# Performance work log

Hardware: AMD Instinct MI355X
Metric: run time of the kernel (lower is better)

The kernel has to match this reference:

```python
import math
import jax, jax.numpy as jnp
import numpy as np

IN_CH = 512
KEY = 512
VAL = 512
B, T = 8, 2048
SQRT_KEY = math.sqrt(float(KEY))


def setup_inputs() -> dict:
    key = jax.random.key(0)
    ks = jax.random.split(key, 7)
    s_in = 1.0 / math.sqrt(IN_CH)
    return {
        "x": jax.random.normal(ks[0], (B, T, IN_CH), dtype=jnp.float32),
        "Wq": jax.random.uniform(ks[1], (IN_CH, KEY), jnp.float32, -s_in, s_in),
        "bq": jax.random.uniform(ks[2], (KEY,), jnp.float32, -s_in, s_in),
        "Wk": jax.random.uniform(ks[3], (IN_CH, KEY), jnp.float32, -s_in, s_in),
        "bk": jax.random.uniform(ks[4], (KEY,), jnp.float32, -s_in, s_in),
        "Wv": jax.random.uniform(ks[5], (IN_CH, VAL), jnp.float32, -s_in, s_in),
        "bv": jax.random.uniform(ks[6], (VAL,), jnp.float32, -s_in, s_in),
    }


def reference(x, Wq, bq, Wk, bk, Wv, bv):
    # x: [B, T, C]
    q = x @ Wq + bq          # [B, T, K]
    k = x @ Wk + bk          # [B, T, K]
    v = x @ Wv + bv          # [B, T, V]
    logits = jnp.einsum("btk,bsk->bts", q, k)  # [B, T(q), T(kv)]
    mask = jnp.tril(jnp.ones((T, T), dtype=bool))  # causal: key s <= query t
    logits = jnp.where(mask[None, :, :], logits, -jnp.inf)
    # NOTE: original torch code softmaxes over dim=1 (the QUERY axis) — kept faithful.
    probs = jax.nn.softmax(logits / SQRT_KEY, axis=1)
    read = jnp.einsum("bts,bsv->btv", probs, v)  # [B, T, V]
    return jnp.concatenate((x, read), axis=2)    # [B, T, C+V]
```

## Files before the change

### kernel.cpp

```cpp
#include <hip/hip_runtime.h>
#include <hip/hip_bf16.h>
#include <math.h>

#define BATCH 8
#define SEQ   2048
#define CH    512
#define ROWS  (BATCH * SEQ)
#define INVSQ 0.044194173824159216f

#define BM 128
#define BK 32
#define TILE_ELEMS (BM * BK)
#define TP 68

typedef __attribute__((ext_vector_type(8))) __bf16 bf16x8;
typedef __attribute__((ext_vector_type(4))) float f32x4;

__device__ inline unsigned short f2bf(float f) {
    unsigned u = __builtin_bit_cast(unsigned, f);
    u += 0x7fffu + ((u >> 16) & 1u);
    return (unsigned short)(u >> 16);
}
__device__ inline float bf2f(unsigned short s) {
    unsigned u = ((unsigned)s) << 16;
    return __builtin_bit_cast(float, u);
}

__device__ __forceinline__ void stage_tile(
    const unsigned short* __restrict__ gbase, size_t stride,
    unsigned short* lds, int wave, int lane)
{
#pragma unroll
    for (int j = 0; j < 2; ++j) {
        int chunk = wave * 2 + j;
        int row = chunk * 16 + (lane >> 2);
        const unsigned short* g = gbase + (size_t)row * stride + ((lane & 3) << 3);
        __builtin_amdgcn_global_load_lds(
            (const __attribute__((address_space(1))) unsigned int*)g,
            (__attribute__((address_space(3))) unsigned int*)(lds + (chunk << 9)),
            16, 0, 0);
    }
}

__device__ __forceinline__ void load_frags(
    const unsigned short* lds, int w0, int l16, int quad, bf16x8* f)
{
#pragma unroll
    for (int r = 0; r < 4; ++r)
        f[r] = *(const bf16x8*)(lds + (w0 + r * 16 + l16) * BK + quad * 8);
}

__global__ __launch_bounds__(256) void fuse_x_kernel(
    const float* __restrict__ x, unsigned short* __restrict__ xb,
    float* __restrict__ out, float* __restrict__ Z)
{
    if (blockIdx.x < 64) Z[blockIdx.x * 256 + threadIdx.x] = 0.f;
    size_t base = ((size_t)blockIdx.x * 256 + threadIdx.x) * 8;
    size_t row = base >> 9, c = base & 511;
    float4 v0 = *(const float4*)(x + base);
    float4 v1 = *(const float4*)(x + base + 4);
    float* o = out + row * 1024 + c;
    *(float4*)o = v0;
    *(float4*)(o + 4) = v1;
    alignas(16) unsigned short t[8];
    t[0] = f2bf(v0.x); t[1] = f2bf(v0.y); t[2] = f2bf(v0.z); t[3] = f2bf(v0.w);
    t[4] = f2bf(v1.x); t[5] = f2bf(v1.y); t[6] = f2bf(v1.z); t[7] = f2bf(v1.w);
    *(uint4*)(xb + base) = *(const uint4*)t;
}

__global__ __launch_bounds__(256) void transpose_w_kernel(
    const float* __restrict__ Wq, const float* __restrict__ Wk,
    const float* __restrict__ Wv, unsigned short* __restrict__ Wt)
{
    __shared__ unsigned short T[64 * TP];
    const int k0 = blockIdx.x * 64, n0 = blockIdx.y * 64, w = blockIdx.z;
    const float* W = (w == 0) ? Wq : (w == 1) ? Wk : Wv;
    const int tid = threadIdx.x;
#pragma unroll
    for (int i = 0; i < 2; ++i) {
        int slot = tid + i * 256;
        int kr = slot >> 3, c8 = (slot & 7) << 3;
        float4 a = *(const float4*)(W + (size_t)(k0 + kr) * CH + n0 + c8);
        float4 b = *(const float4*)(W + (size_t)(k0 + kr) * CH + n0 + c8 + 4);
        T[(c8 + 0) * TP + kr] = f2bf(a.x); T[(c8 + 1) * TP + kr] = f2bf(a.y);
        T[(c8 + 2) * TP + kr] = f2bf(a.z); T[(c8 + 3) * TP + kr] = f2bf(a.w);
        T[(c8 + 4) * TP + kr] = f2bf(b.x); T[(c8 + 5) * TP + kr] = f2bf(b.y);
        T[(c8 + 6) * TP + kr] = f2bf(b.z); T[(c8 + 7) * TP + kr] = f2bf(b.w);
    }
    __syncthreads();
#pragma unroll
    for (int i = 0; i < 2; ++i) {
        int slot = tid + i * 256;
        int nr = slot >> 3, k8 = (slot & 7) << 3;
        uint2 lo = *(const uint2*)(T + nr * TP + k8);
        uint2 hi = *(const uint2*)(T + nr * TP + k8 + 4);
        uint4 u; u.x = lo.x; u.y = lo.y; u.z = hi.x; u.w = hi.y;
        *(uint4*)(Wt + ((size_t)w * CH + n0 + nr) * CH + k0 + k8) = u;
    }
}

__global__ __launch_bounds__(256) void transpose_v_kernel(
    const unsigned short* __restrict__ vb, const float* __restrict__ Z,
    unsigned short* __restrict__ Vt)
{
    __shared__ unsigned short T[64 * TP];
    const int s0 = blockIdx.x * 64, v0 = blockIdx.y * 64, b = blockIdx.z;
    const int tid = threadIdx.x;
#pragma unroll
    for (int i = 0; i < 2; ++i) {
        int slot = tid + i * 256;
        int sr = slot >> 3, c8 = (slot & 7) << 3;
        float inv = 1.0f / Z[b * SEQ + s0 + sr];
        uint4 raw = *(const uint4*)(vb + ((size_t)b * SEQ + s0 + sr) * CH + v0 + c8);
        const unsigned short* p = (const unsigned short*)&raw;
#pragma unroll
        for (int j = 0; j < 8; ++j)
            T[(c8 + j) * TP + sr] = f2bf(bf2f(p[j]) * inv);
    }
    __syncthreads();
#pragma unroll
    for (int i = 0; i < 2; ++i) {
        int slot = tid + i * 256;
        int vr = slot >> 3, s8 = (slot & 7) << 3;
        uint2 lo = *(const uint2*)(T + vr * TP + s8);
        uint2 hi = *(const uint2*)(T + vr * TP + s8 + 4);
        uint4 u; u.x = lo.x; u.y = lo.y; u.z = hi.x; u.w = hi.y;
        *(uint4*)(Vt + ((size_t)b * CH + v0 + vr) * SEQ + s0 + s8) = u;
    }
}

#define MFMA_ROW(r, af) \
    acc[r][0] = __builtin_amdgcn_mfma_f32_16x16x32_bf16(af, b0, acc[r][0], 0, 0, 0); \
    acc[r][1] = __builtin_amdgcn_mfma_f32_16x16x32_bf16(af, b1, acc[r][1], 0, 0, 0); \
    acc[r][2] = __builtin_amdgcn_mfma_f32_16x16x32_bf16(af, b2, acc[r][2], 0, 0, 0); \
    acc[r][3] = __builtin_amdgcn_mfma_f32_16x16x32_bf16(af, b3, acc[r][3], 0, 0, 0);

__global__ __launch_bounds__(512, 2) void qkv8_kernel(
    const unsigned short* __restrict__ xb, const unsigned short* __restrict__ Wt,
    const float* __restrict__ bq, const float* __restrict__ bk,
    const float* __restrict__ bv, unsigned short* __restrict__ qkv)
{
    __shared__ unsigned short lds[24576];
    const int tid = threadIdx.x;
    const int lane = tid & 63, wave = tid >> 6;
    const int waveA = wave >> 2;
    const int waveB = wave & 3;
    const int quad = lane >> 4, l16 = lane & 15;

    int id = (int)blockIdx.x;
    id = (id & 7) * 96 + (id >> 3);
    const int xt = id / 12, wt = id - xt * 12;
    const int xrow0 = xt << 8, wrow0 = wt << 7;

    const unsigned short* __restrict__ Wg = Wt + (size_t)wrow0 * CH;
    const unsigned short* __restrict__ Xg = xb + (size_t)xrow0 * CH;

    const int srow = tid >> 2;
    const int scol = (((tid & 3) ^ ((tid >> 3) & 3)) << 3);
    const size_t ga  = (size_t)srow * CH + scol;
    const size_t gb1 = (size_t)(srow + 128) * CH + scol;
    const int wdst = wave * 512;
    const int rswz = ((quad ^ ((l16 >> 1) & 3)) << 3);
    const int arow = waveA * 64 + l16;
    const int brow = waveB * 64 + l16;

    f32x4 acc[4][4] = {};

    auto stageA = [&](int V) {
        if (V >= 16) return;
        const unsigned short* g = Wg + ga + V * 32;
        unsigned short* d = lds + (V & 1) * 4096 + wdst;
        __builtin_amdgcn_global_load_lds(
            (const __attribute__((address_space(1))) unsigned int*)g,
            (__attribute__((address_space(3))) unsigned int*)d, 16, 0, 0);
    };
    auto stageB = [&](int V) {
        if (V >= 16) return;
        const unsigned short* g0 = Xg + ga + V * 32;
        const unsigned short* g1 = Xg + gb1 + V * 32;
        unsigned short* d = lds + 8192 + (V & 1) * 8192 + wdst;
        __builtin_amdgcn_global_load_lds(
            (const __attribute__((address_space(1))) unsigned int*)g0,
            (__attribute__((address_space(3))) unsigned int*)d, 16, 0, 0);
        __builtin_amdgcn_global_load_lds(
            (const __attribute__((address_space(1))) unsigned int*)g1,
            (__attribute__((address_space(3))) unsigned int*)(d + 4096), 16, 0, 0);
    };

    stageA(0); stageB(0); stageB(1);
    asm volatile("s_waitcnt vmcnt(2)" ::: "memory");
    __builtin_amdgcn_s_barrier();
    __builtin_amdgcn_sched_barrier(0);

#pragma unroll
    for (int U = 0; U < 16; ++U) {
        const unsigned short* Ab = lds + (U & 1) * 4096;
        const unsigned short* Bb = lds + 8192 + (U & 1) * 8192;
        bf16x8 a0, a1, b0, b1, b2, b3;
        b0 = *(const bf16x8*)(Bb + (brow +  0) * 32 + rswz);
        b1 = *(const bf16x8*)(Bb + (brow + 16) * 32 + rswz);
        b2 = *(const bf16x8*)(Bb + (brow + 32) * 32 + rswz);
        b3 = *(const bf16x8*)(Bb + (brow + 48) * 32 + rswz);
        a0 = *(const bf16x8*)(Ab + (arow +  0) * 32 + rswz);
        a1 = *(const bf16x8*)(Ab + (arow + 16) * 32 + rswz);
        stageA(U + 1);
        __builtin_amdgcn_s_barrier();
        asm volatile("s_waitcnt lgkmcnt(0)" ::: "memory");
        __builtin_amdgcn_sched_barrier(0);
        __builtin_amdgcn_s_setprio(1);
        MFMA_ROW(0, a0);
        MFMA_ROW(1, a1);
        __builtin_amdgcn_s_setprio(0);
        __builtin_amdgcn_s_barrier();
        __builtin_amdgcn_sched_barrier(0);
        a0 = *(const bf16x8*)(Ab + (arow + 32) * 32 + rswz);
        a1 = *(const bf16x8*)(Ab + (arow + 48) * 32 + rswz);
        stageB(U + 2);
        __builtin_amdgcn_s_barrier();
        asm volatile("s_waitcnt lgkmcnt(0)" ::: "memory");
        __builtin_amdgcn_sched_barrier(0);
        __builtin_amdgcn_s_setprio(1);
        MFMA_ROW(2, a0);
        MFMA_ROW(3, a1);
        __builtin_amdgcn_s_setprio(0);
        if (U <= 13)      asm volatile("s_waitcnt vmcnt(2)" ::: "memory");
        else if (U == 14) asm volatile("s_waitcnt vmcnt(0)" ::: "memory");
        __builtin_amdgcn_s_barrier();
        __builtin_amdgcn_sched_barrier(0);
    }

    const int which = wrow0 >> 9;
    const float* bias = (which == 0) ? bq : (which == 1) ? bk : bv;
    const float scale = (which == 0) ? INVSQ : 1.0f;
    unsigned short* outw = qkv + (size_t)which * ROWS * CH;
    const int colblk = wrow0 & 511;
#pragma unroll
    for (int r = 0; r < 4; ++r) {
        int colb = colblk + waveA * 64 + r * 16 + quad * 4;
        float4 b4 = *(const float4*)(bias + colb);
#pragma unroll
        for (int c = 0; c < 4; ++c) {
            int m = xrow0 + waveB * 64 + c * 16 + l16;
            alignas(8) unsigned short pk[4];
            pk[0] = f2bf((acc[r][c][0] + b4.x) * scale);
            pk[1] = f2bf((acc[r][c][1] + b4.y) * scale);
            pk[2] = f2bf((acc[r][c][2] + b4.z) * scale);
            pk[3] = f2bf((acc[r][c][3] + b4.w) * scale);
            *(uint2*)(outw + (size_t)m * CH + colb) = *(const uint2*)pk;
        }
    }
}
#undef MFMA_ROW

__global__ __launch_bounds__(256) void logits_kernel(
    const unsigned short* __restrict__ qb, const unsigned short* __restrict__ kb,
    unsigned short* __restrict__ E, float* __restrict__ Z)
{
    __shared__ unsigned short As[2 * TILE_ELEMS];
    __shared__ unsigned short Bs[2 * TILE_ELEMS];
    const int id = blockIdx.x;
    const int b = id & 7;
    const int i = id >> 3;
    int tt = (int)((sqrtf(8.f * (float)i + 1.f) - 1.f) * 0.5f);
    int st = i - ((tt * (tt + 1)) >> 1);
    while (st < 0)  { --tt; st = i - ((tt * (tt + 1)) >> 1); }
    while (st > tt) { ++tt; st = i - ((tt * (tt + 1)) >> 1); }
    const int m0s = st * BM;
    const int n0t = tt * BM;
    const int tid = threadIdx.x;
    const int lane = tid & 63, wave = tid >> 6;
    const int wm = (wave >> 1) * 64, wn = (wave & 1) * 64;
    const int quad = lane >> 4, l16 = lane & 15;
    const unsigned short* kB = kb + (size_t)b * SEQ * CH;
    const unsigned short* qB = qb + (size_t)b * SEQ * CH;

    f32x4 acc[4][4] = {};
    for (int kk = 0; kk < CH; kk += 64) {
        stage_tile(kB + (size_t)m0s * CH + kk,      CH, As,              wave, lane);
        stage_tile(kB + (size_t)m0s * CH + kk + 32, CH, As + TILE_ELEMS, wave, lane);
        stage_tile(qB + (size_t)n0t * CH + kk,      CH, Bs,              wave, lane);
        stage_tile(qB + (size_t)n0t * CH + kk + 32, CH, Bs + TILE_ELEMS, wave, lane);
        __syncthreads();
#pragma unroll
        for (int h = 0; h < 2; ++h) {
            bf16x8 a[4], bb[4];
            load_frags(As + h * TILE_ELEMS, wm, l16, quad, a);
            load_frags(Bs + h * TILE_ELEMS, wn, l16, quad, bb);
#pragma unroll
            for (int r = 0; r < 4; ++r)
#pragma unroll
                for (int c = 0; c < 4; ++c)
                    acc[r][c] = __builtin_amdgcn_mfma_f32_16x16x32_bf16(a[r], bb[c], acc[r][c], 0, 0, 0);
        }
        __syncthreads();
    }
#pragma unroll
    for (int r = 0; r < 4; ++r) {
        int sb = m0s + wm + r * 16 + quad * 4;
        float ev[4][4];
#pragma unroll
        for (int c = 0; c < 4; ++c) {
            int t = n0t + wn + c * 16 + l16;
#pragma unroll
            for (int reg = 0; reg < 4; ++reg)
                ev[c][reg] = (sb + reg <= t) ? __expf(acc[r][c][reg]) : 0.f;
        }
#pragma unroll
        for (int reg = 0; reg < 4; ++reg) {
            float z = ev[0][reg] + ev[1][reg] + ev[2][reg] + ev[3][reg];
            z += __shfl_xor(z, 1);
            z += __shfl_xor(z, 2);
            z += __shfl_xor(z, 4);
            z += __shfl_xor(z, 8);
            if (l16 == 0) atomicAdd(&Z[b * SEQ + sb + reg], z);
        }
#pragma unroll
        for (int c = 0; c < 4; ++c) {
            int t = n0t + wn + c * 16 + l16;
            alignas(8) unsigned short pk[4];
            pk[0] = f2bf(ev[c][0]); pk[1] = f2bf(ev[c][1]);
            pk[2] = f2bf(ev[c][2]); pk[3] = f2bf(ev[c][3]);
            *(uint2*)(E + ((size_t)b * SEQ + t) * SEQ + sb) = *(const uint2*)pk;
        }
    }
}

__global__ __launch_bounds__(256) void read_kernel(
    const unsigned short* __restrict__ E, const unsigned short* __restrict__ Vt,
    float* __restrict__ out)
{
    __shared__ unsigned short As[2 * TILE_ELEMS];
    __shared__ unsigned short Bs[2 * TILE_ELEMS];
    const int id = blockIdx.x;
    const int b = id & 7;
    const int rem = id >> 3;
    const int mv = rem & 3;
    const int r0 = rem >> 2;
    const int tt = (r0 < 8) ? r0 : 23 - r0;
    const int m0v = mv * BM;
    const int n0t = tt * BM;
    const int Kmax = (tt + 1) * BM;
    const int tid = threadIdx.x;
    const int lane = tid & 63, wave = tid >> 6;
    const int wm = (wave >> 1) * 64, wn = (wave & 1) * 64;
    const int quad = lane >> 4, l16 = lane & 15;
    const unsigned short* Vb = Vt + (size_t)b * CH * SEQ;
    const unsigned short* Eb = E + (size_t)b * SEQ * SEQ;

    f32x4 acc[4][4] = {};
    for (int kk = 0; kk < Kmax; kk += 64) {
        stage_tile(Vb + (size_t)m0v * SEQ + kk,      SEQ, As,              wave, lane);
        stage_tile(Vb + (size_t)m0v * SEQ + kk + 32, SEQ, As + TILE_ELEMS, wave, lane);
        stage_tile(Eb + (size_t)n0t * SEQ + kk,      SEQ, Bs,              wave, lane);
        stage_tile(Eb + (size_t)n0t * SEQ + kk + 32, SEQ, Bs + TILE_ELEMS, wave, lane);
        __syncthreads();
#pragma unroll
        for (int h = 0; h < 2; ++h) {
            bf16x8 a[4], bb[4];
            load_frags(As + h * TILE_ELEMS, wm, l16, quad, a);
            load_frags(Bs + h * TILE_ELEMS, wn, l16, quad, bb);
#pragma unroll
            for (int r = 0; r < 4; ++r)
#pragma unroll
                for (int c = 0; c < 4; ++c)
                    acc[r][c] = __builtin_amdgcn_mfma_f32_16x16x32_bf16(a[r], bb[c], acc[r][c], 0, 0, 0);
        }
        __syncthreads();
    }
#pragma unroll
    for (int r = 0; r < 4; ++r) {
        int v = 512 + m0v + wm + r * 16 + quad * 4;
#pragma unroll
        for (int c = 0; c < 4; ++c) {
            int t = n0t + wn + c * 16 + l16;
            float4 f;
            f.x = acc[r][c][0]; f.y = acc[r][c][1];
            f.z = acc[r][c][2]; f.w = acc[r][c][3];
            *(float4*)(out + ((size_t)b * SEQ + t) * 1024 + v) = f;
        }
    }
}

extern "C" void kernel_launch(void* const* d_in, const int* in_sizes, int n_in,
                              void* d_out, int out_size, void* d_ws, size_t ws_size,
                              hipStream_t stream) {
    const float* x  = (const float*)d_in[0];
    const float* Wq = (const float*)d_in[1];
    const float* bq = (const float*)d_in[2];
    const float* Wk = (const float*)d_in[3];
    const float* bk = (const float*)d_in[4];
    const float* Wv = (const float*)d_in[5];
    const float* bv = (const float*)d_in[6];
    float* out = (float*)d_out;

    char* ws = (char*)d_ws;
    const size_t QKV_BYTES = (size_t)ROWS * CH * 2;
    const size_t E_BYTES   = (size_t)BATCH * SEQ * SEQ * 2;
    unsigned short* qkv = (unsigned short*)ws;
    unsigned short* qb = qkv;
    unsigned short* kb = (unsigned short*)(ws + QKV_BYTES);
    unsigned short* vb = (unsigned short*)(ws + 2 * QKV_BYTES);
    unsigned short* E  = (unsigned short*)(ws + 3 * QKV_BYTES);
    float* Z = (float*)(ws + 3 * QKV_BYTES + E_BYTES);
    unsigned short* xb = E;
    unsigned short* Wt = (unsigned short*)((char*)E + QKV_BYTES);
    unsigned short* Vt = qb;

    dim3 blk(256);
    fuse_x_kernel<<<dim3(4096), blk, 0, stream>>>(x, xb, out, Z);
    transpose_w_kernel<<<dim3(8, 8, 3), blk, 0, stream>>>(Wq, Wk, Wv, Wt);
    qkv8_kernel<<<dim3(768), dim3(512), 0, stream>>>(xb, Wt, bq, bk, bv, qkv);
    logits_kernel<<<dim3(1088), blk, 0, stream>>>(qb, kb, E, Z);
    transpose_v_kernel<<<dim3(32, 8, 8), blk, 0, stream>>>(vb, Z, Vt);
    read_kernel<<<dim3(512), blk, 0, stream>>>(E, Vt, out);
}
```

Measured before the change: 230.0 us.

## Port logits kernel to pipelined 8-wave async-LDS GEMM with 128x256 tiles

Replaces the simple 4-wave 128x128 logits GEMM, which stages tiles synchronously, with the same 8-wave, 512-thread pipeline used by the QKV projection. That pipeline uses double-buffered global_load_lds staging, barrier-interleaved MFMA phases and setprio, and covers 128 key rows by 256 query rows. The causal tile enumeration changes to 128x256 blocks, 576 in place of 1088, and the pipeline loop is factored into a shared macro. This aims to hide global-load latency and improve operand reuse in the QK^T stage. The cost is coarser tiles that do more wasted work on the masked triangle, and fewer blocks to spread across the CUs.

```diff
diff --git a/kernel.cpp b/kernel.cpp
--- a/kernel.cpp
+++ b/kernel.cpp
@@ -135,6 +135,48 @@
     acc[r][2] = __builtin_amdgcn_mfma_f32_16x16x32_bf16(af, b2, acc[r][2], 0, 0, 0); \
     acc[r][3] = __builtin_amdgcn_mfma_f32_16x16x32_bf16(af, b3, acc[r][3], 0, 0, 0);
 
+#define PIPELINE_LOOP                                                         \
+    stageA(0); stageB(0); stageB(1);                                          \
+    asm volatile("s_waitcnt vmcnt(2)" ::: "memory");                          \
+    __builtin_amdgcn_s_barrier();                                             \
+    __builtin_amdgcn_sched_barrier(0);                                        \
+    _Pragma("unroll")                                                         \
+    for (int U = 0; U < 16; ++U) {                                            \
+        const unsigned short* Ab = lds + (U & 1) * 4096;                      \
+        const unsigned short* Bb = lds + 8192 + (U & 1) * 8192;               \
+        bf16x8 a0, a1, b0, b1, b2, b3;                                        \
+        b0 = *(const bf16x8*)(Bb + (brow +  0) * 32 + rswz);                  \
+        b1 = *(const bf16x8*)(Bb + (brow + 16) * 32 + rswz);                  \
+        b2 = *(const bf16x8*)(Bb + (brow + 32) * 32 + rswz);                  \
+        b3 = *(const bf16x8*)(Bb + (brow + 48) * 32 + rswz);                  \
+        a0 = *(const bf16x8*)(Ab + (arow +  0) * 32 + rswz);                  \
+        a1 = *(const bf16x8*)(Ab + (arow + 16) * 32 + rswz);                  \
+        stageA(U + 1);                                                        \
+        __builtin_amdgcn_s_barrier();                                         \
+        asm volatile("s_waitcnt lgkmcnt(0)" ::: "memory");                    \
+        __builtin_amdgcn_sched_barrier(0);                                    \
+        __builtin_amdgcn_s_setprio(1);                                        \
+        MFMA_ROW(0, a0);                                                      \
+        MFMA_ROW(1, a1);                                                      \
+        __builtin_amdgcn_s_setprio(0);                                        \
+        __builtin_amdgcn_s_barrier();                                         \
+        __builtin_amdgcn_sched_barrier(0);                                    \
+        a0 = *(const bf16x8*)(Ab + (arow + 32) * 32 + rswz);                  \
+        a1 = *(const bf16x8*)(Ab + (arow + 48) * 32 + rswz);                  \
+        stageB(U + 2);                                                        \
+        __builtin_amdgcn_s_barrier();                                         \
+        asm volatile("s_waitcnt lgkmcnt(0)" ::: "memory");                    \
+        __builtin_amdgcn_sched_barrier(0);                                    \
+        __builtin_amdgcn_s_setprio(1);                                        \
+        MFMA_ROW(2, a0);                                                      \
+        MFMA_ROW(3, a1);                                                      \
+        __builtin_amdgcn_s_setprio(0);                                        \
+        if (U <= 13)      asm volatile("s_waitcnt vmcnt(2)" ::: "memory");    \
+        else if (U == 14) asm volatile("s_waitcnt vmcnt(0)" ::: "memory");    \
+        __builtin_amdgcn_s_barrier();                                         \
+        __builtin_amdgcn_sched_barrier(0);                                    \
+    }
+
 __global__ __launch_bounds__(512, 2) void qkv8_kernel(
     const unsigned short* __restrict__ xb, const unsigned short* __restrict__ Wt,
     const float* __restrict__ bq, const float* __restrict__ bk,
@@ -187,47 +229,7 @@
             (__attribute__((address_space(3))) unsigned int*)(d + 4096), 16, 0, 0);
     };
 
-    stageA(0); stageB(0); stageB(1);
-    asm volatile("s_waitcnt vmcnt(2)" ::: "memory");
-    __builtin_amdgcn_s_barrier();
-    __builtin_amdgcn_sched_barrier(0);
-
-#pragma unroll
-    for (int U = 0; U < 16; ++U) {
-        const unsigned short* Ab = lds + (U & 1) * 4096;
-        const unsigned short* Bb = lds + 8192 + (U & 1) * 8192;
-        bf16x8 a0, a1, b0, b1, b2, b3;
-        b0 = *(const bf16x8*)(Bb + (brow +  0) * 32 + rswz);
-        b1 = *(const bf16x8*)(Bb + (brow + 16) * 32 + rswz);
-        b2 = *(const bf16x8*)(Bb + (brow + 32) * 32 + rswz);
-        b3 = *(const bf16x8*)(Bb + (brow + 48) * 32 + rswz);
-        a0 = *(const bf16x8*)(Ab + (arow +  0) * 32 + rswz);
-        a1 = *(const bf16x8*)(Ab + (arow + 16) * 32 + rswz);
-        stageA(U + 1);
-        __builtin_amdgcn_s_barrier();
-        asm volatile("s_waitcnt lgkmcnt(0)" ::: "memory");
-        __builtin_amdgcn_sched_barrier(0);
-        __builtin_amdgcn_s_setprio(1);
-        MFMA_ROW(0, a0);
-        MFMA_ROW(1, a1);
-        __builtin_amdgcn_s_setprio(0);
-        __builtin_amdgcn_s_barrier();
-        __builtin_amdgcn_sched_barrier(0);
-        a0 = *(const bf16x8*)(Ab + (arow + 32) * 32 + rswz);
-        a1 = *(const bf16x8*)(Ab + (arow + 48) * 32 + rswz);
-        stageB(U + 2);
-        __builtin_amdgcn_s_barrier();
-        asm volatile("s_waitcnt lgkmcnt(0)" ::: "memory");
-        __builtin_amdgcn_sched_barrier(0);
-        __builtin_amdgcn_s_setprio(1);
-        MFMA_ROW(2, a0);
-        MFMA_ROW(3, a1);
-        __builtin_amdgcn_s_setprio(0);
-        if (U <= 13)      asm volatile("s_waitcnt vmcnt(2)" ::: "memory");
-        else if (U == 14) asm volatile("s_waitcnt vmcnt(0)" ::: "memory");
-        __builtin_amdgcn_s_barrier();
-        __builtin_amdgcn_sched_barrier(0);
-    }
+    PIPELINE_LOOP
 
     const int which = wrow0 >> 9;
     const float* bias = (which == 0) ? bq : (which == 1) ? bk : bv;
@@ -250,57 +252,71 @@
         }
     }
 }
-#undef MFMA_ROW
-
-__global__ __launch_bounds__(256) void logits_kernel(
+
+__global__ __launch_bounds__(512, 2) void logits8_kernel(
     const unsigned short* __restrict__ qb, const unsigned short* __restrict__ kb,
     unsigned short* __restrict__ E, float* __restrict__ Z)
 {
-    __shared__ unsigned short As[2 * TILE_ELEMS];
-    __shared__ unsigned short Bs[2 * TILE_ELEMS];
-    const int id = blockIdx.x;
-    const int b = id & 7;
-    const int i = id >> 3;
-    int tt = (int)((sqrtf(8.f * (float)i + 1.f) - 1.f) * 0.5f);
-    int st = i - ((tt * (tt + 1)) >> 1);
-    while (st < 0)  { --tt; st = i - ((tt * (tt + 1)) >> 1); }
-    while (st > tt) { ++tt; st = i - ((tt * (tt + 1)) >> 1); }
-    const int m0s = st * BM;
-    const int n0t = tt * BM;
+    __shared__ unsigned short lds[24576];
     const int tid = threadIdx.x;
     const int lane = tid & 63, wave = tid >> 6;
-    const int wm = (wave >> 1) * 64, wn = (wave & 1) * 64;
+    const int waveA = wave >> 2;
+    const int waveB = wave & 3;
     const int quad = lane >> 4, l16 = lane & 15;
-    const unsigned short* kB = kb + (size_t)b * SEQ * CH;
-    const unsigned short* qB = qb + (size_t)b * SEQ * CH;
+
+    const int b = (int)blockIdx.x & 7;
+    const int i = (int)blockIdx.x >> 3;
+    int tt2 = (int)((sqrtf(4.f * (float)i + 1.f) - 1.f) * 0.5f);
+    int st = i - tt2 * (tt2 + 1);
+    while (st < 0)           { --tt2; st = i - tt2 * (tt2 + 1); }
+    while (st > 2 * tt2 + 1) { ++tt2; st = i - tt2 * (tt2 + 1); }
+    const int m0s = st << 7;
+    const int n0t = tt2 << 8;
+
+    const unsigned short* __restrict__ Wg = kb + ((size_t)b * SEQ + m0s) * CH;
+    const unsigned short* __restrict__ Xg = qb + ((size_t)b * SEQ + n0t) * CH;
+
+    const int srow = tid >> 2;
+    const int scol = (((tid & 3) ^ ((tid >> 3) & 3)) << 3);
+    const size_t ga  = (size_t)srow * CH + scol;
+    const size_t gb1 = (size_t)(srow + 128) * CH + scol;
+    const int wdst = wave * 512;
+    const int rswz = ((quad ^ ((l16 >> 1) & 3)) << 3);
+    const int arow = waveA * 64 + l16;
+    const int brow = waveB * 64 + l16;
 
     f32x4 acc[4][4] = {};
-    for (int kk = 0; kk < CH; kk += 64) {
-        stage_tile(kB + (size_t)m0s * CH + kk,      CH, As,              wave, lane);
-        stage_tile(kB + (size_t)m0s * CH + kk + 32, CH, As + TILE_ELEMS, wave, lane);
-        stage_tile(qB + (size_t)n0t * CH + kk,      CH, Bs,              wave, lane);
-        stage_tile(qB + (size_t)n0t * CH + kk + 32, CH, Bs + TILE_ELEMS, wave, lane);
-        __syncthreads();
-#pragma unroll
-        for (int h = 0; h < 2; ++h) {
-            bf16x8 a[4], bb[4];
-            load_frags(As + h * TILE_ELEMS, wm, l16, quad, a);
-            load_frags(Bs + h * TILE_ELEMS, wn, l16, quad, bb);
-#pragma unroll
-            for (int r = 0; r < 4; ++r)
-#pragma unroll
-                for (int c = 0; c < 4; ++c)
-                    acc[r][c] = __builtin_amdgcn_mfma_f32_16x16x32_bf16(a[r], bb[c], acc[r][c], 0, 0, 0);
-        }
-        __syncthreads();
-    }
+
+    auto stageA = [&](int V) {
+        if (V >= 16) return;
+        const unsigned short* g = Wg + ga + V * 32;
+        unsigned short* d = lds + (V & 1) * 4096 + wdst;
+        __builtin_amdgcn_global_load_lds(
+            (const __attribute__((address_space(1))) unsigned int*)g,
+            (__attribute__((address_space(3))) unsigned int*)d, 16, 0, 0);
+    };
+    auto stageB = [&](int V) {
+        if (V >= 16) return;
+        const unsigned short* g0 = Xg + ga + V * 32;
+        const unsigned short* g1 = Xg + gb1 + V * 32;
+        unsigned short* d = lds + 8192 + (V & 1) * 8192 + wdst;
+        __builtin_amdgcn_global_load_lds(
+            (const __attribute__((address_space(1))) unsigned int*)g0,
+            (__attribute__((address_space(3))) unsigned int*)d, 16, 0, 0);
+        __builtin_amdgcn_global_load_lds(
+            (const __attribute__((address_space(1))) unsigned int*)g1,
+            (__attribute__((address_space(3))) unsigned int*)(d + 4096), 16, 0, 0);
+    };
+
+    PIPELINE_LOOP
+
 #pragma unroll
     for (int r = 0; r < 4; ++r) {
-        int sb = m0s + wm + r * 16 + quad * 4;
+        int sb = m0s + waveA * 64 + r * 16 + quad * 4;
         float ev[4][4];
 #pragma unroll
         for (int c = 0; c < 4; ++c) {
-            int t = n0t + wn + c * 16 + l16;
+            int t = n0t + waveB * 64 + c * 16 + l16;
 #pragma unroll
             for (int reg = 0; reg < 4; ++reg)
                 ev[c][reg] = (sb + reg <= t) ? __expf(acc[r][c][reg]) : 0.f;
@@ -316,7 +332,7 @@
         }
 #pragma unroll
         for (int c = 0; c < 4; ++c) {
-            int t = n0t + wn + c * 16 + l16;
+            int t = n0t + waveB * 64 + c * 16 + l16;
             alignas(8) unsigned short pk[4];
             pk[0] = f2bf(ev[c][0]); pk[1] = f2bf(ev[c][1]);
             pk[2] = f2bf(ev[c][2]); pk[3] = f2bf(ev[c][3]);
@@ -324,6 +340,8 @@
         }
     }
 }
+#undef PIPELINE_LOOP
+#undef MFMA_ROW
 
 __global__ __launch_bounds__(256) void read_kernel(
     const unsigned short* __restrict__ E, const unsigned short* __restrict__ Vt,
@@ -410,7 +428,7 @@
     fuse_x_kernel<<<dim3(4096), blk, 0, stream>>>(x, xb, out, Z);
     transpose_w_kernel<<<dim3(8, 8, 3), blk, 0, stream>>>(Wq, Wk, Wv, Wt);
     qkv8_kernel<<<dim3(768), dim3(512), 0, stream>>>(xb, Wt, bq, bk, bv, qkv);
-    logits_kernel<<<dim3(1088), blk, 0, stream>>>(qb, kb, E, Z);
+    logits8_kernel<<<dim3(576), dim3(512), 0, stream>>>(qb, kb, E, Z);
     transpose_v_kernel<<<dim3(32, 8, 8), blk, 0, stream>>>(vb, Z, Vt);
     read_kernel<<<dim3(512), blk, 0, stream>>>(E, Vt, out);
 }
```

Result: slower. 234.8 us (+2.1%).
